# Kernel optimization log

Hardware: AMD Instinct MI355X
Metric: run time of the kernel (lower is better)

## Reference

```python
import jax, jax.numpy as jnp
import numpy as np

B, IN, OUT, G = 8192, 512, 512, 20


def setup_inputs() -> dict:
    key = jax.random.key(0)
    k1, k2, k3 = jax.random.split(key, 3)
    x = jax.random.normal(k1, (B, IN), dtype=jnp.float32)
    coeffs = jax.random.normal(k2, (OUT, IN, G + 1), dtype=jnp.float32) * 0.1
    base_w = jax.random.normal(k3, (OUT, IN), dtype=jnp.float32) * 0.1
    return {"x": x, "coeffs": coeffs, "base_w": base_w}


def reference(x, coeffs, base_w):
    g = coeffs.shape[-1] - 1  # grid_size
    xc = jnp.clip(x, -1.0, 1.0)
    base = jax.nn.silu(xc) @ base_w.T  # [B, out]
    x_grid = (xc + 1.0) * 0.5 * g  # [B, in], in [0, g]
    idx = jnp.clip(jnp.floor(x_grid).astype(jnp.int32), 0, g - 1)  # [B, in]
    t = x_grid - idx.astype(x.dtype)  # [B, in]
    b, n = x.shape
    bi = jnp.arange(b)[:, None]
    fi = jnp.arange(n)[None, :]
    # Sparse interpolation weights over grid bins: 2 nonzeros per (b, i).
    w = jnp.zeros((b, n, g + 1), dtype=x.dtype)
    w = w.at[bi, fi, idx].add(1.0 - t)
    w = w.at[bi, fi, idx + 1].add(t)  # idx+1 <= g since idx <= g-1
    # y[b,o] = sum_i sum_g w[b,i,g] * coeffs[o,i,g]
    y = jnp.einsum('big,oig->bo', w, coeffs)
    return base + y
```

## Files before the change

kernel.cpp:

```cpp
#include <hip/hip_runtime.h>
#include <stdint.h>


typedef short v8s __attribute__((ext_vector_type(8)));
typedef float v4f __attribute__((ext_vector_type(4)));

#define B_DIM 8192
#define IN_DIM 512
#define OUT_DIM 512
#define G_DIM 20
#define FPT 4
#define KT_TOTAL (IN_DIM / FPT)
#define KSPLIT 3
#define BM 128
#define BN 128
#define CHUNKS 12
#define PLANE 2048
#define TILE_BYTES (CHUNKS * PLANE)

#define P_BYTES ((size_t)IN_DIM * B_DIM * 8)
#define WT_BYTES ((size_t)(OUT_DIM / BN) * KT_TOTAL * TILE_BYTES)
#define PART_ELEMS ((size_t)B_DIM * OUT_DIM)
#define WS_NEED (P_BYTES + WT_BYTES + (size_t)KSPLIT * PART_ELEMS * 2)

#define PACK_BLKS ((B_DIM / 64) * (IN_DIM / 64))
#define WPACK_BLKS ((OUT_DIM * IN_DIM) / 256)

static __device__ __forceinline__ unsigned f2bf(float f) {
  unsigned u = __builtin_bit_cast(unsigned, f);
  return (u + 0x7fffu + ((u >> 16) & 1u)) >> 16;
}

static __device__ __forceinline__ float bflo(unsigned u) {
  return __builtin_bit_cast(float, u << 16);
}
static __device__ __forceinline__ float bfhi(unsigned u) {
  return __builtin_bit_cast(float, u & 0xffff0000u);
}

static __device__ __forceinline__ void lds_barrier() {
  __builtin_amdgcn_sched_barrier(0);
  asm volatile("s_waitcnt lgkmcnt(0)" ::: "memory");
  __builtin_amdgcn_s_barrier();
  __builtin_amdgcn_sched_barrier(0);
}

__global__ void zero_out_kernel(uint4* __restrict__ out) {
  out[(size_t)blockIdx.x * 256 + threadIdx.x] = uint4{0u, 0u, 0u, 0u};
}

__global__ void pack_fused_kernel(const float* __restrict__ x, uint2* __restrict__ P,
                                  const float* __restrict__ coeffs,
                                  const float* __restrict__ base_w,
                                  char* __restrict__ Wt) {
  __shared__ uint2 tile[64 * 65];
  const int t = threadIdx.x;
  if (blockIdx.x < PACK_BLKS) {
    const int b0 = (blockIdx.x & (B_DIM / 64 - 1)) * 64;
    const int i0 = (blockIdx.x / (B_DIM / 64)) * 64;
    const int tr = t >> 6;
    const int tc = t & 63;
#pragma unroll
    for (int it = 0; it < 16; ++it) {
      int br = it * 4 + tr;
      float xv = x[(size_t)(b0 + br) * IN_DIM + i0 + tc];
      float xc = fminf(fmaxf(xv, -1.0f), 1.0f);
      float xg = (xc + 1.0f) * 10.0f;
      int idx = (int)floorf(xg);
      idx = idx < 0 ? 0 : (idx > G_DIM - 1 ? G_DIM - 1 : idx);
      float tt = xg - (float)idx;
      float sl = xc / (1.0f + __expf(-xc));
      uint2 pv;
      pv.x = f2bf(1.0f - tt) | (f2bf(tt) << 16);
      pv.y = (unsigned)idx | (f2bf(sl) << 16);
      tile[tc * 65 + br] = pv;
    }
    __syncthreads();
#pragma unroll
    for (int it = 0; it < 16; ++it) {
      int ir = it * 4 + tr;
      P[(size_t)(i0 + ir) * B_DIM + b0 + tc] = tile[ir * 65 + tc];
    }
  } else {
    const unsigned u = (blockIdx.x - PACK_BLKS) * 256 + t;
    const int s = u >> 9;
    const int w = u & 511;
    const int row = w >> 2;
    const int f = w & 3;
    const int n_blk = s / KT_TOTAL;
    const int kt = s - n_blk * KT_TOTAL;
    const int o = n_blk * 128 + row;
    const int i = kt * 4 + f;
    const size_t g = (size_t)o * IN_DIM + i;
    const float* c = coeffs + g * 21;
    float cf[21];
#pragma unroll
    for (int j = 0; j < 21; ++j) cf[j] = c[j];
    float bw = base_w[g];
    unsigned d[12];
#pragma unroll
    for (int j = 0; j < 10; ++j) d[j] = f2bf(cf[2 * j]) | (f2bf(cf[2 * j + 1]) << 16);
    d[10] = f2bf(cf[20]) | (f2bf(bw) << 16);
    d[11] = 0u;
    char* slab = Wt + (size_t)s * TILE_BYTES;
#pragma unroll
    for (int p = 0; p < 3; ++p)
      *(uint4*)(slab + (3 * f + p) * PLANE + row * 16) =
          uint4{d[4 * p], d[4 * p + 1], d[4 * p + 2], d[4 * p + 3]};
  }
}

__global__ void reduce_kernel(const uint4* __restrict__ p, v4f* __restrict__ out) {
  size_t i = (size_t)blockIdx.x * 256 + threadIdx.x;
  const size_t q = PART_ELEMS / 8;
  uint4 a = p[i], b = p[i + q], c = p[i + 2 * q];
  v4f lo, hi;
  lo[0] = bflo(a.x) + bflo(b.x) + bflo(c.x);
  hi[0] = bfhi(a.x) + bfhi(b.x) + bfhi(c.x);
  lo[1] = bflo(a.y) + bflo(b.y) + bflo(c.y);
  hi[1] = bfhi(a.y) + bfhi(b.y) + bfhi(c.y);
  lo[2] = bflo(a.z) + bflo(b.z) + bflo(c.z);
  hi[2] = bfhi(a.z) + bfhi(b.z) + bfhi(c.z);
  lo[3] = bflo(a.w) + bflo(b.w) + bflo(c.w);
  hi[3] = bfhi(a.w) + bfhi(b.w) + bfhi(c.w);
  v4f o0 = {lo[0], hi[0], lo[1], hi[1]};
  v4f o1 = {lo[2], hi[2], lo[3], hi[3]};
  out[2 * i] = o0;
  out[2 * i + 1] = o1;
}

static __device__ __forceinline__ int slot_off(int slot) {
  return ((slot >> 3) << 11) + ((slot & 7) << 1);
}

template <bool ATOMIC>
__global__ __launch_bounds__(256, 3) void kan_gemm(const uint2* __restrict__ P,
                                                   const char* __restrict__ Wt,
                                                   unsigned short* __restrict__ part,
                                                   float* __restrict__ outA) {
  __shared__ uint4 lds4[TILE_BYTES / 16];
  char* Ab = (char*)lds4;
  const int t = threadIdx.x;
  const int lane = t & 63;
  const int wv = t >> 6;
  const int wm = wv >> 1, wn = wv & 1;

  const int L = blockIdx.x + ((blockIdx.y + (blockIdx.z << 2)) << 6);
  const int nL = (L & 7) * 96 + (L >> 3);
  const int bx = nL & 63;
  const int by = (nL >> 6) & 3;
  const int bz = nL >> 8;

  const int b0 = bx * BM;
  const int n_blk = by;
  const int z = bz;
  const int kt0 = (z * KT_TOTAL) / KSPLIT;
  const int ktend = ((z + 1) * KT_TOTAL) / KSPLIT;

  v4f acc[4][4];
  const v4f z4 = {0.f, 0.f, 0.f, 0.f};
#pragma unroll
  for (int ii = 0; ii < 4; ++ii)
#pragma unroll
    for (int jj = 0; jj < 4; ++jj) acc[ii][jj] = z4;

  {
    const uint4 zz = {0u, 0u, 0u, 0u};
#pragma unroll
    for (int j = 0; j < 6; ++j) lds4[t + 256 * j] = zz;
  }

  char* abase0 = Ab + 3 * wv * PLANE + lane * 16;
  char* abase1 = Ab + 3 * wv * PLANE + (lane + 64) * 16;
  uint2 pv0 = P[(size_t)(kt0 * 4 + wv) * B_DIM + b0 + lane];
  uint2 pv1 = P[(size_t)(kt0 * 4 + wv) * B_DIM + b0 + lane + 64];
  char *c0a, *c0b, *c1a, *c1b;
  {
    int i0x = (int)(pv0.y & 0xffffu);
    c0a = abase0 + slot_off(i0x);
    c0b = abase0 + slot_off(i0x + 1);
    int i1x = (int)(pv1.y & 0xffffu);
    c1a = abase1 + slot_off(i1x);
    c1b = abase1 + slot_off(i1x + 1);
  }

  const int r16 = lane & 15;
  const int q16 = lane >> 4;

  const uint4* wbase = (const uint4*)(Wt + (size_t)n_blk * KT_TOTAL * TILE_BYTES);
  int bidx[3][4];
#pragma unroll
  for (int s = 0; s < 3; ++s)
#pragma unroll
    for (int cn = 0; cn < 4; ++cn)
      bidx[s][cn] = (s * 4 + q16) * 128 + wn * 64 + cn * 16 + r16;

  for (int kt = kt0; kt < ktend; ++kt) {
    lds_barrier();

    const uint4* wsrc = wbase + (size_t)kt * (TILE_BYTES / 16);
    uint4 bv[3][4];
#pragma unroll
    for (int s = 0; s < 3; ++s)
#pragma unroll
      for (int cn = 0; cn < 4; ++cn)
        bv[s][cn] = wsrc[bidx[s][cn]];

    const int ktn = (kt + 1 < ktend) ? kt + 1 : kt;
    uint2 pn0 = P[(size_t)(ktn * 4 + wv) * B_DIM + b0 + lane];
    uint2 pn1 = P[(size_t)(ktn * 4 + wv) * B_DIM + b0 + lane + 64];

    {
      *(unsigned short*)c0a = 0;
      *(unsigned short*)c0b = 0;
      int idx = (int)(pv0.y & 0xffffu);
      char* wa = abase0 + slot_off(idx);
      char* wb = abase0 + slot_off(idx + 1);
      *(unsigned short*)wa = (unsigned short)pv0.x;
      *(unsigned short*)wb = (unsigned short)(pv0.x >> 16);
      *(unsigned short*)(abase0 + 2 * PLANE + 10) = (unsigned short)(pv0.y >> 16);
      c0a = wa; c0b = wb;
    }
    {
      *(unsigned short*)c1a = 0;
      *(unsigned short*)c1b = 0;
      int idx = (int)(pv1.y & 0xffffu);
      char* wa = abase1 + slot_off(idx);
      char* wb = abase1 + slot_off(idx + 1);
      *(unsigned short*)wa = (unsigned short)pv1.x;
      *(unsigned short*)wb = (unsigned short)(pv1.x >> 16);
      *(unsigned short*)(abase1 + 2 * PLANE + 10) = (unsigned short)(pv1.y >> 16);
      c1a = wa; c1b = wb;
    }
    pv0 = pn0;
    pv1 = pn1;

    lds_barrier();

#pragma unroll
    for (int s = 0; s < 3; ++s) {
      const int chunk = s * 4 + q16;
      v8s af[4];
#pragma unroll
      for (int rm = 0; rm < 4; ++rm) {
        int row = wm * 64 + rm * 16 + r16;
        af[rm] = *(const v8s*)(Ab + chunk * PLANE + row * 16);
      }
#pragma unroll
      for (int rm = 0; rm < 4; ++rm)
#pragma unroll
        for (int cn = 0; cn < 4; ++cn)
          acc[rm][cn] = __builtin_amdgcn_mfma_f32_16x16x32_bf16(
              af[rm], __builtin_bit_cast(v8s, bv[s][cn]), acc[rm][cn], 0, 0, 0);
    }
  }

  const int q4 = (lane >> 4) * 4;
  if (ATOMIC) {
#pragma unroll
    for (int rm = 0; rm < 4; ++rm)
#pragma unroll
      for (int cn = 0; cn < 4; ++cn)
#pragma unroll
        for (int r = 0; r < 4; ++r) {
          int row = b0 + wm * 64 + rm * 16 + q4 + r;
          int col = n_blk * BN + wn * 64 + cn * 16 + r16;
          atomicAdd(outA + (size_t)row * OUT_DIM + col, acc[rm][cn][r]);
        }
  } else {
    unsigned short* mypart = part + (size_t)z * PART_ELEMS;
#pragma unroll
    for (int rm = 0; rm < 4; ++rm)
#pragma unroll
      for (int cn = 0; cn < 4; ++cn)
#pragma unroll
        for (int r = 0; r < 4; ++r) {
          int row = b0 + wm * 64 + rm * 16 + q4 + r;
          int col = n_blk * BN + wn * 64 + cn * 16 + r16;
          mypart[(size_t)row * OUT_DIM + col] = (unsigned short)f2bf(acc[rm][cn][r]);
        }
  }
}

extern "C" void kernel_launch(void* const* d_in, const int* in_sizes, int n_in,
                              void* d_out, int out_size, void* d_ws, size_t ws_size,
                              hipStream_t stream) {
  const float* x = (const float*)d_in[0];
  const float* coeffs = (const float*)d_in[1];
  const float* base_w = (const float*)d_in[2];
  float* out = (float*)d_out;

  uint2* P = (uint2*)d_ws;
  char* Wt = (char*)d_ws + P_BYTES;
  unsigned short* part = (unsigned short*)((char*)d_ws + P_BYTES + WT_BYTES);

  pack_fused_kernel<<<PACK_BLKS + WPACK_BLKS, 256, 0, stream>>>(x, P, coeffs, base_w, Wt);

  if (ws_size >= WS_NEED) {
    kan_gemm<false><<<dim3(B_DIM / BM, OUT_DIM / BN, KSPLIT), 256, 0, stream>>>(P, Wt, part, out);
    reduce_kernel<<<(int)(PART_ELEMS / 8 / 256), 256, 0, stream>>>((const uint4*)part, (v4f*)out);
  } else {
    zero_out_kernel<<<(int)((PART_ELEMS * 4) / 4096), 256, 0, stream>>>((uint4*)out);
    kan_gemm<true><<<dim3(B_DIM / BM, OUT_DIM / BN, KSPLIT), 256, 0, stream>>>(P, Wt, part, out);
  }
}
```

Baseline: 177.0 us.

## Double-buffer LDS A-tile staging and raise MFMA wave priority

Doubles the LDS A-operand buffer so the sparse interpolation weights for the next k-step are scattered into one buffer while MFMAs read the other. This cuts the two barriers per iteration to one. It also wraps the MFMA block in s_setprio to favour the matrix work. LDS use per block doubles to about 48KB, which may cut occupancy below the launch_bounds target of 3 blocks per CU.

Measured after the change: 179.3 us. About the same (+1.3%).

```diff
diff --git a/kernel.cpp b/kernel.cpp
--- a/kernel.cpp
+++ b/kernel.cpp
@@ -138,7 +138,7 @@
                                                    const char* __restrict__ Wt,
                                                    unsigned short* __restrict__ part,
                                                    float* __restrict__ outA) {
-  __shared__ uint4 lds4[TILE_BYTES / 16];
+  __shared__ uint4 lds4[2 * TILE_BYTES / 16];
   char* Ab = (char*)lds4;
   const int t = threadIdx.x;
   const int lane = t & 63;
@@ -167,21 +167,30 @@
   {
     const uint4 zz = {0u, 0u, 0u, 0u};
 #pragma unroll
-    for (int j = 0; j < 6; ++j) lds4[t + 256 * j] = zz;
-  }
-
-  char* abase0 = Ab + 3 * wv * PLANE + lane * 16;
-  char* abase1 = Ab + 3 * wv * PLANE + (lane + 64) * 16;
+    for (int j = 0; j < 12; ++j) lds4[t + 256 * j] = zz;
+  }
+
+  const int ro0 = 3 * wv * PLANE + lane * 16;
+  const int ro1 = 3 * wv * PLANE + (lane + 64) * 16;
+
+  char* stg = Ab;
+  char* rd = Ab + TILE_BYTES;
+
   uint2 pv0 = P[(size_t)(kt0 * 4 + wv) * B_DIM + b0 + lane];
   uint2 pv1 = P[(size_t)(kt0 * 4 + wv) * B_DIM + b0 + lane + 64];
-  char *c0a, *c0b, *c1a, *c1b;
+
+  char *cc0a, *cc0b, *cc1a, *cc1b, *ca0a, *ca0b, *ca1a, *ca1b;
   {
     int i0x = (int)(pv0.y & 0xffffu);
-    c0a = abase0 + slot_off(i0x);
-    c0b = abase0 + slot_off(i0x + 1);
+    cc0a = stg + ro0 + slot_off(i0x);
+    cc0b = stg + ro0 + slot_off(i0x + 1);
     int i1x = (int)(pv1.y & 0xffffu);
-    c1a = abase1 + slot_off(i1x);
-    c1b = abase1 + slot_off(i1x + 1);
+    cc1a = stg + ro1 + slot_off(i1x);
+    cc1b = stg + ro1 + slot_off(i1x + 1);
+    ca0a = rd + ro0 + slot_off(0);
+    ca0b = rd + ro0 + slot_off(1);
+    ca1a = rd + ro1 + slot_off(0);
+    ca1b = rd + ro1 + slot_off(1);
   }
 
   const int r16 = lane & 15;
@@ -195,9 +204,52 @@
     for (int cn = 0; cn < 4; ++cn)
       bidx[s][cn] = (s * 4 + q16) * 128 + wn * 64 + cn * 16 + r16;
 
+#define STAGE(ktnext_clamped)                                                   \
+  {                                                                             \
+    uint2 pn0 = P[(size_t)((ktnext_clamped) * 4 + wv) * B_DIM + b0 + lane];     \
+    uint2 pn1 = P[(size_t)((ktnext_clamped) * 4 + wv) * B_DIM + b0 + lane + 64];\
+    *(unsigned short*)cc0a = 0;                                                 \
+    *(unsigned short*)cc0b = 0;                                                 \
+    {                                                                           \
+      int idx = (int)(pv0.y & 0xffffu);                                         \
+      char* wa = stg + ro0 + slot_off(idx);                                     \
+      char* wb = stg + ro0 + slot_off(idx + 1);                                 \
+      *(unsigned short*)wa = (unsigned short)pv0.x;                             \
+      *(unsigned short*)wb = (unsigned short)(pv0.x >> 16);                     \
+      *(unsigned short*)(stg + ro0 + 2 * PLANE + 10) =                          \
+          (unsigned short)(pv0.y >> 16);                                        \
+      cc0a = wa; cc0b = wb;                                                     \
+    }                                                                           \
+    *(unsigned short*)cc1a = 0;                                                 \
+    *(unsigned short*)cc1b = 0;                                                 \
+    {                                                                           \
+      int idx = (int)(pv1.y & 0xffffu);                                         \
+      char* wa = stg + ro1 + slot_off(idx);                                     \
+      char* wb = stg + ro1 + slot_off(idx + 1);                                 \
+      *(unsigned short*)wa = (unsigned short)pv1.x;                             \
+      *(unsigned short*)wb = (unsigned short)(pv1.x >> 16);                     \
+      *(unsigned short*)(stg + ro1 + 2 * PLANE + 10) =                          \
+          (unsigned short)(pv1.y >> 16);                                        \
+      cc1a = wa; cc1b = wb;                                                     \
+    }                                                                           \
+    pv0 = pn0;                                                                  \
+    pv1 = pn1;                                                                  \
+  }
+
+#define SWAPP(a, b) { char* _tmp = a; a = b; b = _tmp; }
+#define SWAP_BUFS()                                                             \
+  {                                                                             \
+    SWAPP(stg, rd);                                                             \
+    SWAPP(cc0a, ca0a); SWAPP(cc0b, ca0b);                                       \
+    SWAPP(cc1a, ca1a); SWAPP(cc1b, ca1b);                                       \
+  }
+
+  lds_barrier();
+  STAGE(kt0 + 1 < ktend ? kt0 + 1 : kt0);
+  SWAP_BUFS();
+  lds_barrier();
+
   for (int kt = kt0; kt < ktend; ++kt) {
-    lds_barrier();
-
     const uint4* wsrc = wbase + (size_t)kt * (TILE_BYTES / 16);
     uint4 bv[3][4];
 #pragma unroll
@@ -206,36 +258,9 @@
       for (int cn = 0; cn < 4; ++cn)
         bv[s][cn] = wsrc[bidx[s][cn]];
 
-    const int ktn = (kt + 1 < ktend) ? kt + 1 : kt;
-    uint2 pn0 = P[(size_t)(ktn * 4 + wv) * B_DIM + b0 + lane];
-    uint2 pn1 = P[(size_t)(ktn * 4 + wv) * B_DIM + b0 + lane + 64];
-
-    {
-      *(unsigned short*)c0a = 0;
-      *(unsigned short*)c0b = 0;
-      int idx = (int)(pv0.y & 0xffffu);
-      char* wa = abase0 + slot_off(idx);
-      char* wb = abase0 + slot_off(idx + 1);
-      *(unsigned short*)wa = (unsigned short)pv0.x;
-      *(unsigned short*)wb = (unsigned short)(pv0.x >> 16);
-      *(unsigned short*)(abase0 + 2 * PLANE + 10) = (unsigned short)(pv0.y >> 16);
-      c0a = wa; c0b = wb;
+    if (kt + 1 < ktend) {
+      STAGE(kt + 2 < ktend ? kt + 2 : kt + 1);
     }
-    {
-      *(unsigned short*)c1a = 0;
-      *(unsigned short*)c1b = 0;
-      int idx = (int)(pv1.y & 0xffffu);
-      char* wa = abase1 + slot_off(idx);
-      char* wb = abase1 + slot_off(idx + 1);
-      *(unsigned short*)wa = (unsigned short)pv1.x;
-      *(unsigned short*)wb = (unsigned short)(pv1.x >> 16);
-      *(unsigned short*)(abase1 + 2 * PLANE + 10) = (unsigned short)(pv1.y >> 16);
-      c1a = wa; c1b = wb;
-    }
-    pv0 = pn0;
-    pv1 = pn1;
-
-    lds_barrier();
 
 #pragma unroll
     for (int s = 0; s < 3; ++s) {
@@ -244,16 +269,24 @@
 #pragma unroll
       for (int rm = 0; rm < 4; ++rm) {
         int row = wm * 64 + rm * 16 + r16;
-        af[rm] = *(const v8s*)(Ab + chunk * PLANE + row * 16);
+        af[rm] = *(const v8s*)(rd + chunk * PLANE + row * 16);
       }
+      __builtin_amdgcn_s_setprio(1);
 #pragma unroll
       for (int rm = 0; rm < 4; ++rm)
 #pragma unroll
         for (int cn = 0; cn < 4; ++cn)
           acc[rm][cn] = __builtin_amdgcn_mfma_f32_16x16x32_bf16(
               af[rm], __builtin_bit_cast(v8s, bv[s][cn]), acc[rm][cn], 0, 0, 0);
+      __builtin_amdgcn_s_setprio(0);
     }
-  }
+
+    lds_barrier();
+    SWAP_BUFS();
+  }
+#undef STAGE
+#undef SWAPP
+#undef SWAP_BUFS
 
   const int q4 = (lane >> 4) * 4;
   if (ATOMIC) {
```

## Build sparse A fragments in registers instead of LDS scatter

Applied to the files above, without the earlier changes.

Removes the shared-memory A tile and its two barriers per K step. Each lane now loads the packed (weight, index) entries for its rows straight from global memory and builds the bf16 MFMA A operand in registers from the bin index. The B loads move into the per-subchunk loop, and s_setprio is raised around the MFMA groups. The cost is redundant global loads of P across lanes and waves and extra ALU select logic per fragment.

Measured after the change: 254.6 us. 43.8% more time.

```diff
diff --git a/kernel.cpp b/kernel.cpp
--- a/kernel.cpp
+++ b/kernel.cpp
@@ -36,13 +36,6 @@
 }
 static __device__ __forceinline__ float bfhi(unsigned u) {
   return __builtin_bit_cast(float, u & 0xffff0000u);
-}
-
-static __device__ __forceinline__ void lds_barrier() {
-  __builtin_amdgcn_sched_barrier(0);
-  asm volatile("s_waitcnt lgkmcnt(0)" ::: "memory");
-  __builtin_amdgcn_s_barrier();
-  __builtin_amdgcn_sched_barrier(0);
 }
 
 __global__ void zero_out_kernel(uint4* __restrict__ out) {
@@ -129,17 +122,11 @@
   out[2 * i + 1] = o1;
 }
 
-static __device__ __forceinline__ int slot_off(int slot) {
-  return ((slot >> 3) << 11) + ((slot & 7) << 1);
-}
-
 template <bool ATOMIC>
 __global__ __launch_bounds__(256, 3) void kan_gemm(const uint2* __restrict__ P,
                                                    const char* __restrict__ Wt,
                                                    unsigned short* __restrict__ part,
                                                    float* __restrict__ outA) {
-  __shared__ uint4 lds4[TILE_BYTES / 16];
-  char* Ab = (char*)lds4;
   const int t = threadIdx.x;
   const int lane = t & 63;
   const int wv = t >> 6;
@@ -164,26 +151,6 @@
 #pragma unroll
     for (int jj = 0; jj < 4; ++jj) acc[ii][jj] = z4;
 
-  {
-    const uint4 zz = {0u, 0u, 0u, 0u};
-#pragma unroll
-    for (int j = 0; j < 6; ++j) lds4[t + 256 * j] = zz;
-  }
-
-  char* abase0 = Ab + 3 * wv * PLANE + lane * 16;
-  char* abase1 = Ab + 3 * wv * PLANE + (lane + 64) * 16;
-  uint2 pv0 = P[(size_t)(kt0 * 4 + wv) * B_DIM + b0 + lane];
-  uint2 pv1 = P[(size_t)(kt0 * 4 + wv) * B_DIM + b0 + lane + 64];
-  char *c0a, *c0b, *c1a, *c1b;
-  {
-    int i0x = (int)(pv0.y & 0xffffu);
-    c0a = abase0 + slot_off(i0x);
-    c0b = abase0 + slot_off(i0x + 1);
-    int i1x = (int)(pv1.y & 0xffffu);
-    c1a = abase1 + slot_off(i1x);
-    c1b = abase1 + slot_off(i1x + 1);
-  }
-
   const int r16 = lane & 15;
   const int q16 = lane >> 4;
 
@@ -195,63 +162,53 @@
     for (int cn = 0; cn < 4; ++cn)
       bidx[s][cn] = (s * 4 + q16) * 128 + wn * 64 + cn * 16 + r16;
 
+  int fArr[3], pArr[3];
+#pragma unroll
+  for (int s = 0; s < 3; ++s) {
+    const int c = s * 4 + q16;
+    fArr[s] = (c * 11) >> 5;
+    pArr[s] = c - 3 * fArr[s];
+  }
+
   for (int kt = kt0; kt < ktend; ++kt) {
-    lds_barrier();
-
     const uint4* wsrc = wbase + (size_t)kt * (TILE_BYTES / 16);
-    uint4 bv[3][4];
-#pragma unroll
-    for (int s = 0; s < 3; ++s)
-#pragma unroll
-      for (int cn = 0; cn < 4; ++cn)
-        bv[s][cn] = wsrc[bidx[s][cn]];
-
-    const int ktn = (kt + 1 < ktend) ? kt + 1 : kt;
-    uint2 pn0 = P[(size_t)(ktn * 4 + wv) * B_DIM + b0 + lane];
-    uint2 pn1 = P[(size_t)(ktn * 4 + wv) * B_DIM + b0 + lane + 64];
-
-    {
-      *(unsigned short*)c0a = 0;
-      *(unsigned short*)c0b = 0;
-      int idx = (int)(pv0.y & 0xffffu);
-      char* wa = abase0 + slot_off(idx);
-      char* wb = abase0 + slot_off(idx + 1);
-      *(unsigned short*)wa = (unsigned short)pv0.x;
-      *(unsigned short*)wb = (unsigned short)(pv0.x >> 16);
-      *(unsigned short*)(abase0 + 2 * PLANE + 10) = (unsigned short)(pv0.y >> 16);
-      c0a = wa; c0b = wb;
-    }
-    {
-      *(unsigned short*)c1a = 0;
-      *(unsigned short*)c1b = 0;
-      int idx = (int)(pv1.y & 0xffffu);
-      char* wa = abase1 + slot_off(idx);
-      char* wb = abase1 + slot_off(idx + 1);
-      *(unsigned short*)wa = (unsigned short)pv1.x;
-      *(unsigned short*)wb = (unsigned short)(pv1.x >> 16);
-      *(unsigned short*)(abase1 + 2 * PLANE + 10) = (unsigned short)(pv1.y >> 16);
-      c1a = wa; c1b = wb;
-    }
-    pv0 = pn0;
-    pv1 = pn1;
-
-    lds_barrier();
-
 #pragma unroll
     for (int s = 0; s < 3; ++s) {
-      const int chunk = s * 4 + q16;
-      v8s af[4];
+      const int f = fArr[s];
+      const int p = pArr[s];
+      const uint2* psrc = P + ((size_t)(kt * 4 + f) << 13) + b0 + wm * 64 + r16;
+      uint2 pvv[4];
+#pragma unroll
+      for (int rm = 0; rm < 4; ++rm) pvv[rm] = psrc[rm * 16];
+      uint4 bvv[4];
+#pragma unroll
+      for (int cn = 0; cn < 4; ++cn) bvv[cn] = wsrc[bidx[s][cn]];
+
 #pragma unroll
       for (int rm = 0; rm < 4; ++rm) {
-        int row = wm * 64 + rm * 16 + r16;
-        af[rm] = *(const v8s*)(Ab + chunk * PLANE + row * 16);
-      }
-#pragma unroll
-      for (int rm = 0; rm < 4; ++rm)
+        const unsigned pvx = pvv[rm].x;
+        const unsigned pvs = pvx >> 16;
+        const int idxr = (int)(pvv[rm].y & 0xffffu) - 8 * p;
+        const int odd = idxr & 1;
+        const int d1 = idxr >> 1;
+        const int d2 = (idxr + 1) >> 1;
+        const unsigned v1 = odd ? (pvx << 16) : pvx;
+        const bool has1 = ((unsigned)idxr <= 7u);
+        const bool has2 = odd && ((unsigned)(idxr + 1) <= 7u);
+        const unsigned silu2 = (p == 2) ? (pvv[rm].y & 0xffff0000u) : 0u;
+        uint4 ad;
+        ad.x = ((has1 && d1 == 0) ? v1 : 0u) | ((has2 && d2 == 0) ? pvs : 0u);
+        ad.y = ((has1 && d1 == 1) ? v1 : 0u) | ((has2 && d2 == 1) ? pvs : 0u);
+        ad.z = ((has1 && d1 == 2) ? v1 : 0u) | ((has2 && d2 == 2) ? pvs : 0u) | silu2;
+        ad.w = ((has1 && d1 == 3) ? v1 : 0u) | ((has2 && d2 == 3) ? pvs : 0u);
+        const v8s af = __builtin_bit_cast(v8s, ad);
+        __builtin_amdgcn_s_setprio(1);
 #pragma unroll
         for (int cn = 0; cn < 4; ++cn)
           acc[rm][cn] = __builtin_amdgcn_mfma_f32_16x16x32_bf16(
-              af[rm], __builtin_bit_cast(v8s, bv[s][cn]), acc[rm][cn], 0, 0, 0);
+              af, __builtin_bit_cast(v8s, bvv[cn]), acc[rm][cn], 0, 0, 0);
+        __builtin_amdgcn_s_setprio(0);
+      }
     }
   }
 
```
